# Kernel tuning notes

Measured on AMD Instinct MI355X. Metric: run time of the kernel, lower is better.

The kernel has to match this reference:

```python
import jax, jax.numpy as jnp
import numpy as np

SCALAR_DIM = 64
VECTOR_DIM = 32
SPIN = 2
N_NODES = 50000
N_EDGES = 1600000
GEO_DIM = 3
IN_DIM = 2 * SCALAR_DIM + VECTOR_DIM + GEO_DIM  # 163
HID = SCALAR_DIM + VECTOR_DIM  # 96


def setup_inputs() -> dict:
    key = jax.random.key(0)
    ks = jax.random.split(key, 9)
    h_scalar = jax.random.normal(ks[0], (N_NODES, SCALAR_DIM), dtype=jnp.float32)
    h_vector = jax.random.normal(ks[1], (N_NODES, VECTOR_DIM), dtype=jnp.float32)
    edge_index = jax.random.randint(ks[2], (2, N_EDGES), 0, N_NODES, dtype=jnp.int64)
    pos = jax.random.normal(ks[3], (N_NODES, 2), dtype=jnp.float32)
    orientation = jax.random.uniform(ks[4], (N_NODES, 1), dtype=jnp.float32)
    # MLP params (Linear: y = x @ W.T + b; store as [in, out] for jnp)
    lim1 = 1.0 / np.sqrt(IN_DIM)
    lim2 = 1.0 / np.sqrt(HID)
    W1 = jax.random.uniform(ks[5], (IN_DIM, HID), minval=-lim1, maxval=lim1, dtype=jnp.float32)
    b1 = jax.random.uniform(ks[6], (HID,), minval=-lim1, maxval=lim1, dtype=jnp.float32)
    W2 = jax.random.uniform(ks[7], (HID, HID), minval=-lim2, maxval=lim2, dtype=jnp.float32)
    b2 = jax.random.uniform(ks[8], (HID,), minval=-lim2, maxval=lim2, dtype=jnp.float32)
    return dict(h_scalar=h_scalar, h_vector=h_vector, edge_index=edge_index,
                pos=pos, orientation=orientation, W1=W1, b1=b1, W2=W2, b2=b2)


def reference(h_scalar, h_vector, edge_index, pos, orientation, W1, b1, W2, b2):
    src, dst = edge_index[0], edge_index[1]
    delta_pos = pos[src] - pos[dst]                         # [E,2]
    dist = jnp.linalg.norm(delta_pos, axis=1, keepdims=True) + 1e-6  # [E,1]
    phi_global = jnp.arctan2(delta_pos[:, 1], delta_pos[:, 0])       # [E]
    alpha_i = orientation[dst, 0]                           # [E]
    delta_phi = phi_global - alpha_i
    geo_feat = jnp.concatenate([dist,
                                jnp.cos(SPIN * delta_phi)[:, None],
                                jnp.sin(SPIN * delta_phi)[:, None]], axis=-1)  # [E,3]
    beta_j = orientation[src, 0]
    rot_angle = (beta_j - alpha_i) * SPIN
    c, s = jnp.cos(rot_angle), jnp.sin(rot_angle)
    R = jnp.stack([jnp.stack([c, -s], -1), jnp.stack([s, c], -1)], axis=-2)  # [E,2,2]
    num_vecs = VECTOR_DIM // 2
    v_j = h_vector[src].reshape(-1, num_vecs, 2)            # [E,V/2,2]
    v_j_rot = jnp.einsum('eij,evj->evi', R, v_j).reshape(-1, VECTOR_DIM)
    msg_input = jnp.concatenate([h_scalar[src], h_scalar[dst], v_j_rot, geo_feat], axis=-1)
    h = jax.nn.silu(msg_input @ W1 + b1)
    raw_msg = h @ W2 + b2                                   # [E, S+V]
    msg_scalar = raw_msg[:, :SCALAR_DIM]
    msg_vector = raw_msg[:, SCALAR_DIM:]
    out_scalar = jax.ops.segment_sum(msg_scalar, dst, num_segments=N_NODES)
    out_vector = jax.ops.segment_sum(msg_vector, dst, num_segments=N_NODES)
    return h_scalar + out_scalar, h_vector + out_vector
```

## Files before the change

### kernel.cpp

```cpp
#include <hip/hip_runtime.h>
#include <hip/hip_bf16.h>

#define N_NODESC 50000
#define N_EDGESC 1600000
#define SDIM 64
#define VDIM 32
#define HID 96
#define IN_DIMC 163

#define GRID_E 6250
#define TPB_E 4
#define NXCD 8
#define XQ (GRID_E / NXCD)
#define XR (GRID_E % NXCD)

typedef float f32x4 __attribute__((ext_vector_type(4)));
typedef short s16x8 __attribute__((ext_vector_type(8)));

__device__ __forceinline__ float bf2f(__hip_bfloat16 x) { return __bfloat162float(x); }
__device__ __forceinline__ __hip_bfloat16 f2bf(float x) { return __float2bfloat16(x); }
__device__ __forceinline__ float bfbits2f(short b) {
    unsigned u = ((unsigned)(unsigned short)b) << 16;
    return __builtin_bit_cast(float, u);
}
__device__ __forceinline__ short f2bfbits(float x) {
    __hip_bfloat16 h = __float2bfloat16(x);
    return *(const short*)&h;
}

__global__ void detect_zero(const int* ei, int* flag, int* __restrict__ counts) {
    int i = blockIdx.x * blockDim.x + threadIdx.x;
    if (i < N_NODESC) counts[i] = 0;
    if (i == 0) {
        int z = 1;
        for (int k = 0; k < 64; ++k) {
            if (ei[2 * k + 1] != 0) { z = 0; break; }
        }
        *flag = z;
    }
}

__global__ void fused_init(const float* __restrict__ hs, const float* __restrict__ hv,
                           float* __restrict__ out, int* __restrict__ counts,
                           const float* __restrict__ W1, const float* __restrict__ W2,
                           __hip_bfloat16* __restrict__ SrcRec,
                           __hip_bfloat16* __restrict__ WbT2,
                           __hip_bfloat16* __restrict__ W1cgT,
                           __hip_bfloat16* __restrict__ W2Tb,
                           const int* __restrict__ ei, const int* __restrict__ flag64) {
    int i = blockIdx.x * blockDim.x + threadIdx.x;
    if (i < N_NODESC * (SDIM + VDIM) / 4) {
        const int HS4 = N_NODESC * SDIM / 4;
        float4 v = (i < HS4) ? ((const float4*)hs)[i] : ((const float4*)hv)[i - HS4];
        ((float4*)out)[i] = v;
    }
    if (i < N_NODESC * VDIM / 8) {
        int n = i >> 2, c = i & 3;
        const float4* hv4 = (const float4*)hv;
        float4 a = hv4[n * 8 + c * 2];
        float4 bq = hv4[n * 8 + c * 2 + 1];
        s16x8 o;
        o[0] = f2bfbits(a.x);  o[1] = f2bfbits(a.y);
        o[2] = f2bfbits(a.z);  o[3] = f2bfbits(a.w);
        o[4] = f2bfbits(bq.x); o[5] = f2bfbits(bq.y);
        o[6] = f2bfbits(bq.z); o[7] = f2bfbits(bq.w);
        *(s16x8*)&SrcRec[n * 128 + 96 + c * 8] = o;
    }
    if (i < 192 * 64) {
        int n = i >> 6, k = i & 63;
        float val = (n < 96) ? W1[k * HID + n] : W1[(64 + k) * HID + (n - 96)];
        WbT2[i] = f2bf(val);
    }
    if (i < 96 * 64) {
        int n = i >> 6, k = i & 63;
        float val = 0.f;
        if (k < 32) val = W1[(128 + k) * HID + n];
        else if (k < 35) val = W1[(160 + (k - 32)) * HID + n];
        W1cgT[i] = f2bf(val);
    }
    if (i < 96 * 96) {
        int n = i / 96, k = i - (i / 96) * 96;
        W2Tb[i] = f2bf(W2[k * HID + n]);
    }
    {
        int dN;
        if (*flag64) dN = (int)((const long long*)ei)[N_EDGESC + i];
        else dN = ei[N_EDGESC + i];
        atomicAdd(&counts[dN], 1);
    }
}

__global__ __launch_bounds__(256, 2) void node_precompute_mfma(
    const float* __restrict__ hs, const __hip_bfloat16* __restrict__ WbT2,
    const float* __restrict__ b1,
    __hip_bfloat16* __restrict__ SrcRec, __hip_bfloat16* __restrict__ Qt) {
    __shared__ __hip_bfloat16 sA[64][72];
    __shared__ __hip_bfloat16 sOut[64][200];
    const int t = threadIdx.x;
    const int lane = t & 63;
    const int w = t >> 6;
    const int m16 = lane & 15;
    const int q = lane >> 4;
    const int nb = blockIdx.x * 64;

    for (int idx = t; idx < 64 * 64; idx += 256) {
        int node = idx >> 6, f = idx & 63;
        int g = nb + node;
        sA[node][f] = f2bf(g < N_NODESC ? hs[g * SDIM + f] : 0.f);
    }
    __syncthreads();

    s16x8 bfr[3][2];
    float b1v[3];
    for (int nt = 0; nt < 3; ++nt) {
        int n_out = w * 48 + nt * 16 + m16;
        for (int kt = 0; kt < 2; ++kt)
            bfr[nt][kt] = *(const s16x8*)&WbT2[n_out * 64 + kt * 32 + q * 8];
        b1v[nt] = (n_out < 96) ? b1[n_out] : 0.f;
    }

    for (int ms = 0; ms < 4; ++ms) {
        s16x8 afr[2];
        for (int kt = 0; kt < 2; ++kt)
            afr[kt] = *(const s16x8*)&sA[ms * 16 + m16][kt * 32 + q * 8];
        f32x4 acc[3];
        for (int nt = 0; nt < 3; ++nt) acc[nt] = (f32x4){0.f, 0.f, 0.f, 0.f};
        for (int nt = 0; nt < 3; ++nt)
            for (int kt = 0; kt < 2; ++kt)
                acc[nt] = __builtin_amdgcn_mfma_f32_16x16x32_bf16(
                    afr[kt], bfr[nt][kt], acc[nt], 0, 0, 0);
        for (int nt = 0; nt < 3; ++nt) {
            int n_out = w * 48 + nt * 16 + m16;
            for (int r = 0; r < 4; ++r)
                sOut[ms * 16 + q * 4 + r][n_out] = f2bf(acc[nt][r] + b1v[nt]);
        }
    }
    __syncthreads();

    for (int idx = t; idx < 64 * 12; idx += 256) {
        int node = idx / 12, ch = idx - (idx / 12) * 12;
        int g = nb + node;
        if (g < N_NODESC)
            *(s16x8*)&SrcRec[g * 128 + ch * 8] = *(const s16x8*)&sOut[node][ch * 8];
    }
    for (int idx = t; idx < 64 * 12; idx += 256) {
        int node = idx / 12, ch = idx - (idx / 12) * 12;
        int g = nb + node;
        if (g < N_NODESC)
            *(s16x8*)&Qt[g * 96 + ch * 8] = *(const s16x8*)&sOut[node][96 + ch * 8];
    }
}

__global__ __launch_bounds__(1024) void scan_kernel(
    const int* __restrict__ counts, int* __restrict__ cur) {
    __shared__ int part[1024];
    const int t = threadIdx.x;
    const int CH = (N_NODESC + 1023) / 1024;
    int lo = t * CH;
    int hi = lo + CH; if (hi > N_NODESC) hi = N_NODESC;
    int s = 0;
    for (int i = lo; i < hi; ++i) s += counts[i];
    part[t] = s;
    __syncthreads();
    for (int d = 1; d < 1024; d <<= 1) {
        int v = (t >= d) ? part[t - d] : 0;
        __syncthreads();
        part[t] += v;
        __syncthreads();
    }
    int run = (t == 0) ? 0 : part[t - 1];
    for (int i = lo; i < hi; ++i) {
        int c = counts[i];
        cur[i] = run;
        run += c;
    }
}

__global__ __launch_bounds__(256) void scatter_kernel(
    const int* __restrict__ ei, const int* __restrict__ flag64,
    int* __restrict__ cur, int2* __restrict__ edges) {
    int e = blockIdx.x * blockDim.x + threadIdx.x;
    if (e >= N_EDGESC) return;
    int sN, dN;
    if (*flag64) {
        const long long* e64 = (const long long*)ei;
        sN = (int)e64[e]; dN = (int)e64[N_EDGESC + e];
    } else { sN = ei[e]; dN = ei[N_EDGESC + e]; }
    int p = atomicAdd(&cur[dN], 1);
    edges[p] = make_int2(sN, dN);
}

__global__ __launch_bounds__(256, 3) void edge_kernel_sorted(
    const int2* __restrict__ edges,
    const float* __restrict__ pos, const float* __restrict__ ori,
    const __hip_bfloat16* __restrict__ W2Tb, const float* __restrict__ b2,
    const __hip_bfloat16* __restrict__ SrcRec, const __hip_bfloat16* __restrict__ Qt,
    const __hip_bfloat16* __restrict__ W1cgT,
    float* __restrict__ out) {
    __shared__ int s_srcM[2][64], s_dstM[2][64];
    __shared__ alignas(16) __hip_bfloat16 hVG[64][72];
    __shared__ alignas(16) __hip_bfloat16 s_vf[64][104];
    __shared__ alignas(16) short sW2f[18 * 64 * 8];
    __shared__ int s_segstart[66];

    const int t = threadIdx.x;
    const int lane = t & 63;
    const int w = t >> 6;
    const int m16 = lane & 15;
    const int q = lane >> 4;
    const int el = t >> 2;
    const int quad = t & 3;
    const int eM = w * 16 + m16;

    if (w == 0) {
        for (int f = 0; f < 18; ++f) {
            int nt = f / 3, kt = f - (f / 3) * 3;
            *(s16x8*)&sW2f[(f * 64 + lane) * 8] =
                *(const s16x8*)&W2Tb[(nt * 16 + m16) * 96 + kt * 32 + q * 8];
        }
    }
    s16x8 bfrC[6][2];
    #pragma unroll
    for (int nt = 0; nt < 6; ++nt)
        #pragma unroll
        for (int kt = 0; kt < 2; ++kt)
            bfrC[nt][kt] = *(const s16x8*)&W1cgT[(nt * 16 + m16) * 64 + kt * 32 + q * 8];
    float b2v[6];
    #pragma unroll
    for (int nt = 0; nt < 6; ++nt) b2v[nt] = b2[nt * 16 + m16];

    int b = blockIdx.x;
    int xcd = b & 7, bi = b >> 3;
    int c = (xcd < XR) ? (xcd * (XQ + 1) + bi)
                       : (XR * (XQ + 1) + (xcd - XR) * XQ + bi);
    const int tile0 = c * TPB_E;

    int2 edT1;
    s16x8 hvvT;
    float rcT, rsT;
    float gdT, gcgT, gsgT;
    {
        int2 edT = edges[tile0 * 64 + el];
        edT1 = edges[(tile0 + 1) * 64 + el];
        hvvT = *(const s16x8*)&SrcRec[edT.x * 128 + 96 + quad * 8];
        int sN = edT.x, dN = edT.y;
        float ca, sa, cb, sb;
        __sincosf(2.0f * ori[dN], &sa, &ca);
        __sincosf(2.0f * ori[sN], &sb, &cb);
        rcT = cb * ca + sb * sa;
        rsT = sb * ca - cb * sa;
        float dx = pos[2 * sN] - pos[2 * dN];
        float dy = pos[2 * sN + 1] - pos[2 * dN + 1];
        float d2 = dx * dx + dy * dy;
        gdT = sqrtf(d2) + 1e-6f;
        float c2f, s2f;
        if (d2 > 0.f) {
            float inv = 1.0f / d2;
            c2f = (dx * dx - dy * dy) * inv;
            s2f = 2.0f * dx * dy * inv;
        } else { c2f = 1.0f; s2f = 0.0f; }
        gcgT = c2f * ca + s2f * sa;
        gsgT = s2f * ca - c2f * sa;
        if (quad == 0) { s_srcM[0][el] = sN; s_dstM[0][el] = dN; }
    }
    __syncthreads();
    s16x8 pqP[3], pqQ[3];
    {
        int sN = s_srcM[0][eM], dN = s_dstM[0][eM];
        #pragma unroll
        for (int kt = 0; kt < 3; ++kt) {
            pqP[kt] = *(const s16x8*)&SrcRec[sN * 128 + kt * 32 + q * 8];
            pqQ[kt] = *(const s16x8*)&Qt[dN * 96 + kt * 32 + q * 8];
        }
    }

    int cur = 0;
    for (int tl = 0; tl < TPB_E; ++tl) {
        const int nx = cur ^ 1;
        const int tlN2 = (tl + 2 < TPB_E) ? tl + 2 : TPB_E - 1;

        {
            s16x8 rv;
            #pragma unroll
            for (int p2 = 0; p2 < 4; ++p2) {
                float x = bfbits2f(hvvT[2 * p2]), y = bfbits2f(hvvT[2 * p2 + 1]);
                rv[2 * p2]     = f2bfbits(rcT * x - rsT * y);
                rv[2 * p2 + 1] = f2bfbits(rsT * x + rcT * y);
            }
            *(s16x8*)&hVG[el][quad * 8] = rv;
            s16x8 up = (s16x8){0, 0, 0, 0, 0, 0, 0, 0};
            if (quad == 0) {
                up[0] = f2bfbits(gdT); up[1] = f2bfbits(gcgT); up[2] = f2bfbits(gsgT);
            }
            *(s16x8*)&hVG[el][32 + quad * 8] = up;
        }
        int2 edT2 = edges[(tile0 + tlN2) * 64 + el];
        s16x8 hvvN = *(const s16x8*)&SrcRec[edT1.x * 128 + 96 + quad * 8];
        {
            s16x8 afr0 = *(const s16x8*)&hVG[eM][q * 8];
            s16x8 afr1 = *(const s16x8*)&hVG[eM][32 + q * 8];
            #pragma unroll
            for (int nt = 0; nt < 6; ++nt) {
                f32x4 a1 = __builtin_amdgcn_mfma_f32_16x16x32_bf16(
                    afr0, bfrC[nt][0], (f32x4){0.f, 0.f, 0.f, 0.f}, 0, 0, 0);
                a1 = __builtin_amdgcn_mfma_f32_16x16x32_bf16(
                    afr1, bfrC[nt][1], a1, 0, 0, 0);
                int u = nt * 16 + m16;
                #pragma unroll
                for (int r = 0; r < 4; ++r)
                    s_vf[w * 16 + q * 4 + r][u] = f2bf(a1[r]);
            }
        }
        float rcN, rsN, gdN, gcgN, gsgN;
        {
            int sN = edT1.x, dN = edT1.y;
            float ca, sa, cb, sb;
            __sincosf(2.0f * ori[dN], &sa, &ca);
            __sincosf(2.0f * ori[sN], &sb, &cb);
            rcN = cb * ca + sb * sa;
            rsN = sb * ca - cb * sa;
            float dx = pos[2 * sN] - pos[2 * dN];
            float dy = pos[2 * sN + 1] - pos[2 * dN + 1];
            float d2 = dx * dx + dy * dy;
            gdN = sqrtf(d2) + 1e-6f;
            float c2f, s2f;
            if (d2 > 0.f) {
                float inv = 1.0f / d2;
                c2f = (dx * dx - dy * dy) * inv;
                s2f = 2.0f * dx * dy * inv;
            } else { c2f = 1.0f; s2f = 0.0f; }
            gcgN = c2f * ca + s2f * sa;
            gsgN = s2f * ca - c2f * sa;
            if (quad == 0) { s_srcM[nx][el] = sN; s_dstM[nx][el] = dN; }
        }

        s16x8 afr[3];
        #pragma unroll
        for (int kt = 0; kt < 3; ++kt) {
            int j = kt * 32 + q * 8;
            s16x8 Vv = *(const s16x8*)&s_vf[eM][j];
            s16x8 hb;
            #pragma unroll
            for (int k2 = 0; k2 < 8; ++k2) {
                float pre = bfbits2f(pqP[kt][k2]) + bfbits2f(pqQ[kt][k2])
                          + bfbits2f(Vv[k2]);
                float h = pre / (1.0f + __expf(-pre));
                hb[k2] = f2bfbits(h);
            }
            afr[kt] = hb;
        }
        {
            int sN = s_srcM[nx][eM], dN = s_dstM[nx][eM];
            #pragma unroll
            for (int kt = 0; kt < 3; ++kt) {
                pqP[kt] = *(const s16x8*)&SrcRec[sN * 128 + kt * 32 + q * 8];
                pqQ[kt] = *(const s16x8*)&Qt[dN * 96 + kt * 32 + q * 8];
            }
        }
        {
            f32x4 acc[6];
            #pragma unroll
            for (int nt = 0; nt < 6; ++nt) acc[nt] = (f32x4){0.f, 0.f, 0.f, 0.f};
            #pragma unroll
            for (int nt = 0; nt < 6; ++nt)
                #pragma unroll
                for (int kt = 0; kt < 3; ++kt) {
                    s16x8 bf = *(const s16x8*)&sW2f[((nt * 3 + kt) * 64 + lane) * 8];
                    acc[nt] = __builtin_amdgcn_mfma_f32_16x16x32_bf16(
                        afr[kt], bf, acc[nt], 0, 0, 0);
                }
            #pragma unroll
            for (int nt = 0; nt < 6; ++nt) {
                int u = nt * 16 + m16;
                float bb = b2v[nt];
                #pragma unroll
                for (int r = 0; r < 4; ++r)
                    s_vf[w * 16 + q * 4 + r][u] = f2bf(acc[nt][r] + bb);
            }
        }
        __syncthreads();

        {
            int dl = s_dstM[cur][lane];
            int dp = (lane > 0) ? s_dstM[cur][lane - 1] : -1;
            bool bnd = (lane > 0) && (dl != dp);
            unsigned long long mask = __ballot(bnd);
            int nseg = (int)__popcll(mask) + 1;
            if (bnd) s_segstart[__popcll(mask & (~0ull >> (63 - lane)))] = lane;
            if (lane == 0) s_segstart[0] = 0;

            for (int idx = t; idx < nseg * HID; idx += 256) {
                int sg = idx / HID;
                int u = idx - sg * HID;
                int e0 = s_segstart[sg];
                int e1 = (sg + 1 < nseg) ? s_segstart[sg + 1] : 64;
                float sum = 0.f;
                for (int e = e0; e < e1; ++e) sum += bf2f(s_vf[e][u]);
                int dN = s_dstM[cur][e0];
                if (u < SDIM) atomicAdd(&out[dN * SDIM + u], sum);
                else atomicAdd(&out[N_NODESC * SDIM + dN * VDIM + (u - SDIM)], sum);
            }
        }

        edT1 = edT2; hvvT = hvvN;
        rcT = rcN; rsT = rsN; gdT = gdN; gcgT = gcgN; gsgT = gsgN;
        cur = nx;
        __syncthreads();
    }
}

__global__ __launch_bounds__(128) void node_precompute(
    const float* __restrict__ hs, const float* __restrict__ hv,
    const float* __restrict__ W1, const float* __restrict__ b1,
    __hip_bfloat16* __restrict__ Pp, __hip_bfloat16* __restrict__ Qt,
    __hip_bfloat16* __restrict__ Ut, __hip_bfloat16* __restrict__ Vt) {
    int n = blockIdx.x;
    __shared__ float s_hs[SDIM];
    __shared__ float s_hv[VDIM];
    int t = threadIdx.x;
    if (t < 64) s_hs[t] = hs[n * SDIM + t];
    else if (t < 96) s_hv[t - 64] = hv[n * VDIM + (t - 64)];
    __syncthreads();
    if (t < HID) {
        float p = b1[t], qq = 0.f, u = 0.f, v = 0.f;
        for (int k = 0; k < 64; ++k) {
            float x = s_hs[k];
            p += x * W1[k * HID + t];
            qq += x * W1[(64 + k) * HID + t];
        }
        for (int pr = 0; pr < 16; ++pr) {
            float x = s_hv[2 * pr], y = s_hv[2 * pr + 1];
            float wa = W1[(128 + 2 * pr) * HID + t];
            float wb = W1[(128 + 2 * pr + 1) * HID + t];
            u += x * wa + y * wb;
            v += x * wb - y * wa;
        }
        Pp[n * HID + t] = f2bf(p);
        Qt[n * HID + t] = f2bf(qq);
        Ut[n * HID + t] = f2bf(u);
        Vt[n * HID + t] = f2bf(v);
    }
}

__global__ void init_out(const float* __restrict__ hs, const float* __restrict__ hv,
                         float* __restrict__ out) {
    int i = blockIdx.x * blockDim.x + threadIdx.x;
    if (i >= N_NODESC * (SDIM + VDIM)) return;
    out[i] = (i < N_NODESC * SDIM) ? hs[i] : hv[i - N_NODESC * SDIM];
}

__global__ void detect_kernel(const int* ei, int* flag) {
    if (blockIdx.x == 0 && threadIdx.x == 0) {
        int z = 1;
        for (int k = 0; k < 64; ++k) {
            if (ei[2 * k + 1] != 0) { z = 0; break; }
        }
        *flag = z;
    }
}

__global__ __launch_bounds__(256) void edge_kernel(
    const int* __restrict__ ei, const float* __restrict__ pos,
    const float* __restrict__ ori, const float* __restrict__ W1,
    const float* __restrict__ W2, const float* __restrict__ b2,
    const __hip_bfloat16* __restrict__ Pp, const __hip_bfloat16* __restrict__ Qt,
    const __hip_bfloat16* __restrict__ Ut, const __hip_bfloat16* __restrict__ Vt,
    const int* __restrict__ flag64, float* __restrict__ out) {
    __shared__ int s_src[64], s_dst[64];
    __shared__ float s_c[64], s_s[64], s_d[64], s_cg[64], s_sg[64];
    __shared__ float s_w1d[3][HID];
    __shared__ __hip_bfloat16 hA[64][104];
    __shared__ __hip_bfloat16 W2T[HID][104];

    const int t = threadIdx.x;
    const int lane = t & 63;
    const int w = t >> 6;
    const int m16 = lane & 15;
    const int q = lane >> 4;

    for (int idx = t; idx < HID * HID; idx += 256) {
        int k = idx / HID;
        int n = idx - k * HID;
        W2T[n][k] = f2bf(W2[idx]);
    }
    for (int idx = t; idx < 3 * HID; idx += 256) {
        int r = idx / HID, j = idx - r * HID;
        s_w1d[r][j] = W1[(160 + r) * HID + j];
    }
    __syncthreads();

    s16x8 bfr[6][3];
    for (int nt = 0; nt < 6; ++nt)
        for (int kt = 0; kt < 3; ++kt)
            bfr[nt][kt] = *(const s16x8*)&W2T[nt * 16 + m16][kt * 32 + q * 8];
    float b2v[6];
    for (int nt = 0; nt < 6; ++nt) b2v[nt] = b2[nt * 16 + m16];

    const bool i64 = (*flag64 != 0);
    const long long* ei64 = (const long long*)ei;

    for (int tile = blockIdx.x; tile < N_EDGESC / 64; tile += gridDim.x) {
        __syncthreads();

        if (t < 64) {
            int e = tile * 64 + t;
            int sN, dN;
            if (i64) { sN = (int)ei64[e]; dN = (int)ei64[N_EDGESC + e]; }
            else     { sN = ei[e];        dN = ei[N_EDGESC + e]; }
            s_src[t] = sN; s_dst[t] = dN;
            float ca, sa, cb, sb;
            __sincosf(2.0f * ori[dN], &sa, &ca);
            __sincosf(2.0f * ori[sN], &sb, &cb);
            s_c[t] = cb * ca + sb * sa;
            s_s[t] = sb * ca - cb * sa;
            float dx = pos[2 * sN] - pos[2 * dN];
            float dy = pos[2 * sN + 1] - pos[2 * dN + 1];
            float d2 = dx * dx + dy * dy;
            s_d[t] = sqrtf(d2) + 1e-6f;
            float c2f, s2f;
            if (d2 > 0.f) {
                float inv = 1.0f / d2;
                c2f = (dx * dx - dy * dy) * inv;
                s2f = 2.0f * dx * dy * inv;
            } else { c2f = 1.0f; s2f = 0.0f; }
            s_cg[t] = c2f * ca + s2f * sa;
            s_sg[t] = s2f * ca - c2f * sa;
        }
        __syncthreads();

        for (int p = 0; p < 24; ++p) {
            int idx = p * 256 + t;
            int e = idx / HID;
            int j = idx - e * HID;
            int sN = s_src[e], dN = s_dst[e];
            float pre = bf2f(Pp[sN * HID + j]) + bf2f(Qt[dN * HID + j])
                      + s_c[e] * bf2f(Ut[sN * HID + j])
                      + s_s[e] * bf2f(Vt[sN * HID + j])
                      + s_d[e] * s_w1d[0][j] + s_cg[e] * s_w1d[1][j]
                      + s_sg[e] * s_w1d[2][j];
            float h = pre / (1.0f + __expf(-pre));
            hA[e][j] = f2bf(h);
        }
        __syncthreads();

        f32x4 acc[6];
        for (int nt = 0; nt < 6; ++nt) acc[nt] = (f32x4){0.f, 0.f, 0.f, 0.f};
        s16x8 afr[3];
        for (int kt = 0; kt < 3; ++kt)
            afr[kt] = *(const s16x8*)&hA[w * 16 + m16][kt * 32 + q * 8];
        for (int nt = 0; nt < 6; ++nt)
            for (int kt = 0; kt < 3; ++kt)
                acc[nt] = __builtin_amdgcn_mfma_f32_16x16x32_bf16(
                    afr[kt], bfr[nt][kt], acc[nt], 0, 0, 0);

        for (int nt = 0; nt < 6; ++nt) {
            int u = nt * 16 + m16;
            for (int r = 0; r < 4; ++r) {
                int eloc = w * 16 + q * 4 + r;
                int dN = s_dst[eloc];
                float val = acc[nt][r] + b2v[nt];
                if (u < SDIM) atomicAdd(&out[dN * SDIM + u], val);
                else atomicAdd(&out[N_NODESC * SDIM + dN * VDIM + (u - SDIM)], val);
            }
        }
    }
}

__global__ __launch_bounds__(192) void edge_fallback(
    const int* __restrict__ ei, const float* __restrict__ hs,
    const float* __restrict__ hv, const float* __restrict__ pos,
    const float* __restrict__ ori, const float* __restrict__ W1,
    const float* __restrict__ b1, const float* __restrict__ W2,
    const float* __restrict__ b2, const int* __restrict__ flag64,
    float* __restrict__ out) {
    __shared__ float s_msg[IN_DIMC];
    __shared__ float s_h[HID];
    int e = blockIdx.x;
    int t = threadIdx.x;
    const bool i64 = (*flag64 != 0);
    int sN, dN;
    if (i64) {
        const long long* e64 = (const long long*)ei;
        sN = (int)e64[e]; dN = (int)e64[N_EDGESC + e];
    } else { sN = ei[e]; dN = ei[N_EDGESC + e]; }

    if (t < IN_DIMC) {
        if (t < 64) s_msg[t] = hs[sN * SDIM + t];
        else if (t < 128) s_msg[t] = hs[dN * SDIM + (t - 64)];
        else {
            float ca, sa, cb, sb;
            __sincosf(2.0f * ori[dN], &sa, &ca);
            __sincosf(2.0f * ori[sN], &sb, &cb);
            float c = cb * ca + sb * sa;
            float s = sb * ca - cb * sa;
            float dx = pos[2 * sN] - pos[2 * dN];
            float dy = pos[2 * sN + 1] - pos[2 * dN + 1];
            float d2 = dx * dx + dy * dy;
            if (t < 160) {
                int pr = (t - 128) >> 1;
                float x = hv[sN * VDIM + 2 * pr], y = hv[sN * VDIM + 2 * pr + 1];
                s_msg[t] = ((t & 1) == 0) ? (c * x - s * y) : (s * x + c * y);
            } else if (t == 160) s_msg[t] = sqrtf(d2) + 1e-6f;
            else {
                float c2f = 1.0f, s2f = 0.0f;
                if (d2 > 0.f) {
                    float inv = 1.0f / d2;
                    c2f = (dx * dx - dy * dy) * inv;
                    s2f = 2.0f * dx * dy * inv;
                }
                s_msg[t] = (t == 161) ? (c2f * ca + s2f * sa) : (s2f * ca - c2f * sa);
            }
        }
    }
    __syncthreads();
    if (t < HID) {
        float a = b1[t];
        for (int k = 0; k < IN_DIMC; ++k) a += s_msg[k] * W1[k * HID + t];
        s_h[t] = a / (1.0f + __expf(-a));
    }
    __syncthreads();
    if (t < HID) {
        float a = b2[t];
        for (int k = 0; k < HID; ++k) a += s_h[k] * W2[k * HID + t];
        if (t < SDIM) atomicAdd(&out[dN * SDIM + t], a);
        else atomicAdd(&out[N_NODESC * SDIM + dN * VDIM + (t - SDIM)], a);
    }
}

extern "C" void kernel_launch(void* const* d_in, const int* in_sizes, int n_in,
                              void* d_out, int out_size, void* d_ws, size_t ws_size,
                              hipStream_t stream) {
    const float* hs  = (const float*)d_in[0];
    const float* hv  = (const float*)d_in[1];
    const int*   ei  = (const int*)d_in[2];
    const float* pos = (const float*)d_in[3];
    const float* ori = (const float*)d_in[4];
    const float* W1  = (const float*)d_in[5];
    const float* b1  = (const float*)d_in[6];
    const float* W2  = (const float*)d_in[7];
    const float* b2  = (const float*)d_in[8];
    float* out = (float*)d_out;

    const size_t SREC = (size_t)N_NODESC * 128 * sizeof(__hip_bfloat16);
    const size_t QTB  = (size_t)N_NODESC * 96 * sizeof(__hip_bfloat16);
    const size_t CNT  = ((size_t)N_NODESC * sizeof(int) + 255) & ~255ull;
    const size_t EDG  = (size_t)N_EDGESC * sizeof(int2);
    const size_t WBT2 = ((size_t)192 * 64 * 2 + 255) & ~255ull;
    const size_t W1CG = ((size_t)96 * 64 * 2 + 255) & ~255ull;
    const size_t W2TS = ((size_t)96 * 96 * 2 + 255) & ~255ull;
    const size_t SORT_WS = SREC + QTB + 2 * CNT + EDG + WBT2 + W1CG + W2TS + 256;

    const size_t TBL = (size_t)N_NODESC * HID * sizeof(__hip_bfloat16);
    const bool big = ws_size >= 4 * TBL + 16;
    const bool srt = ws_size >= SORT_WS;

    if (srt) {
        char* ws = (char*)d_ws;
        __hip_bfloat16* SrcRec = (__hip_bfloat16*)(ws);
        __hip_bfloat16* Qt     = (__hip_bfloat16*)(ws + SREC);
        int* counts            = (int*)(ws + SREC + QTB);
        int* cur               = (int*)(ws + SREC + QTB + CNT);
        int2* edges            = (int2*)(ws + SREC + QTB + 2 * CNT);
        __hip_bfloat16* WbT2   = (__hip_bfloat16*)(ws + SREC + QTB + 2 * CNT + EDG);
        __hip_bfloat16* W1cgT  = (__hip_bfloat16*)(ws + SREC + QTB + 2 * CNT + EDG + WBT2);
        __hip_bfloat16* W2Tb   = (__hip_bfloat16*)(ws + SREC + QTB + 2 * CNT + EDG + WBT2 + W1CG);
        int* flag              = (int*)(ws + SREC + QTB + 2 * CNT + EDG + WBT2 + W1CG + W2TS);

        detect_zero<<<(N_NODESC + 255) / 256, 256, 0, stream>>>(ei, flag, counts);
        fused_init<<<N_EDGESC / 256, 256, 0, stream>>>(
            hs, hv, out, counts, W1, W2, SrcRec, WbT2, W1cgT, W2Tb, ei, flag);
        scan_kernel<<<1, 1024, 0, stream>>>(counts, cur);
        scatter_kernel<<<N_EDGESC / 256, 256, 0, stream>>>(ei, flag, cur, edges);
        node_precompute_mfma<<<(N_NODESC + 63) / 64, 256, 0, stream>>>(
            hs, WbT2, b1, SrcRec, Qt);
        edge_kernel_sorted<<<GRID_E, 256, 0, stream>>>(edges, pos, ori, W2Tb, b2,
                                                       SrcRec, Qt, W1cgT, out);
    } else if (big) {
        char* ws = (char*)d_ws;
        __hip_bfloat16* Pp = (__hip_bfloat16*)(ws);
        __hip_bfloat16* Qt = (__hip_bfloat16*)(ws + TBL);
        __hip_bfloat16* Ut = (__hip_bfloat16*)(ws + 2 * TBL);
        __hip_bfloat16* Vt = (__hip_bfloat16*)(ws + 3 * TBL);
        int* flag = (int*)(ws + 4 * TBL);
        init_out<<<(N_NODESC * (SDIM + VDIM) + 255) / 256, 256, 0, stream>>>(hs, hv, out);
        detect_kernel<<<1, 64, 0, stream>>>(ei, flag);
        node_precompute<<<N_NODESC, 128, 0, stream>>>(hs, hv, W1, b1, Pp, Qt, Ut, Vt);
        edge_kernel<<<2500, 256, 0, stream>>>(ei, pos, ori, W1, W2, b2,
                                              Pp, Qt, Ut, Vt, flag, out);
    } else {
        int* flag = (int*)d_ws;
        init_out<<<(N_NODESC * (SDIM + VDIM) + 255) / 256, 256, 0, stream>>>(hs, hv, out);
        detect_kernel<<<1, 64, 0, stream>>>(ei, flag);
        edge_fallback<<<N_EDGESC, 192, 0, stream>>>(ei, hs, hv, pos, ori, W1, b1,
                                                    W2, b2, flag, out);
    }
}
```

Before: 589.5 us.

## Parallelize prefix scan across blocks and fuse scatter with node precompute

Replaces the single-block serial-chunk prefix scan over node counts with a three-kernel block-parallel scan (per-block partials, scan of block sums, apply offsets). Merges the edge scatter kernel and the node MFMA precompute into one launch, with separate block ranges doing each job so they can run concurrently. Also swaps two divisions in the edge kernel for the hardware reciprocal intrinsic. Adds two kernel launches for the scan and uses slightly less precise reciprocals.

```diff
diff --git a/kernel.cpp b/kernel.cpp
--- a/kernel.cpp
+++ b/kernel.cpp
@@ -13,6 +13,8 @@
 #define NXCD 8
 #define XQ (GRID_E / NXCD)
 #define XR (GRID_E % NXCD)
+#define NPRE 782
+#define SCB 196
 
 typedef float f32x4 __attribute__((ext_vector_type(4)));
 typedef short s16x8 __attribute__((ext_vector_type(8)));
@@ -90,18 +92,74 @@
     }
 }
 
-__global__ __launch_bounds__(256, 2) void node_precompute_mfma(
+__global__ __launch_bounds__(256) void scan_partials(
+    const int* __restrict__ counts, int* __restrict__ cur, int* __restrict__ bsum) {
+    __shared__ int sc[256];
+    const int b = blockIdx.x, t = threadIdx.x;
+    const int i = b * 256 + t;
+    int val = (i < N_NODESC) ? counts[i] : 0;
+    sc[t] = val;
+    __syncthreads();
+    for (int d = 1; d < 256; d <<= 1) {
+        int v = (t >= d) ? sc[t - d] : 0;
+        __syncthreads();
+        sc[t] += v;
+        __syncthreads();
+    }
+    if (i < N_NODESC) cur[i] = sc[t] - val;
+    if (t == 255) bsum[b] = sc[255];
+}
+
+__global__ __launch_bounds__(256) void scan_bsums(
+    const int* __restrict__ bsum, int* __restrict__ boff) {
+    __shared__ int sc[256];
+    const int t = threadIdx.x;
+    int val = (t < SCB) ? bsum[t] : 0;
+    sc[t] = val;
+    __syncthreads();
+    for (int d = 1; d < 256; d <<= 1) {
+        int v = (t >= d) ? sc[t - d] : 0;
+        __syncthreads();
+        sc[t] += v;
+        __syncthreads();
+    }
+    if (t < SCB) boff[t] = sc[t] - val;
+}
+
+__global__ __launch_bounds__(256) void scan_apply(
+    int* __restrict__ cur, const int* __restrict__ boff) {
+    const int i = blockIdx.x * 256 + threadIdx.x;
+    if (i < N_NODESC) cur[i] += boff[blockIdx.x];
+}
+
+__global__ __launch_bounds__(256, 2) void scatter_precompute(
+    const int* __restrict__ ei, const int* __restrict__ flag64,
+    int* __restrict__ cur, int2* __restrict__ edges,
     const float* __restrict__ hs, const __hip_bfloat16* __restrict__ WbT2,
     const float* __restrict__ b1,
     __hip_bfloat16* __restrict__ SrcRec, __hip_bfloat16* __restrict__ Qt) {
     __shared__ __hip_bfloat16 sA[64][72];
     __shared__ __hip_bfloat16 sOut[64][200];
+    const int blk = blockIdx.x;
     const int t = threadIdx.x;
+
+    if (blk >= NPRE) {
+        int e = (blk - NPRE) * 256 + t;
+        int sN, dN;
+        if (*flag64) {
+            const long long* e64 = (const long long*)ei;
+            sN = (int)e64[e]; dN = (int)e64[N_EDGESC + e];
+        } else { sN = ei[e]; dN = ei[N_EDGESC + e]; }
+        int p = atomicAdd(&cur[dN], 1);
+        edges[p] = make_int2(sN, dN);
+        return;
+    }
+
     const int lane = t & 63;
     const int w = t >> 6;
     const int m16 = lane & 15;
     const int q = lane >> 4;
-    const int nb = blockIdx.x * 64;
+    const int nb = blk * 64;
 
     for (int idx = t; idx < 64 * 64; idx += 256) {
         int node = idx >> 6, f = idx & 63;
@@ -149,45 +207,6 @@
         if (g < N_NODESC)
             *(s16x8*)&Qt[g * 96 + ch * 8] = *(const s16x8*)&sOut[node][96 + ch * 8];
     }
-}
-
-__global__ __launch_bounds__(1024) void scan_kernel(
-    const int* __restrict__ counts, int* __restrict__ cur) {
-    __shared__ int part[1024];
-    const int t = threadIdx.x;
-    const int CH = (N_NODESC + 1023) / 1024;
-    int lo = t * CH;
-    int hi = lo + CH; if (hi > N_NODESC) hi = N_NODESC;
-    int s = 0;
-    for (int i = lo; i < hi; ++i) s += counts[i];
-    part[t] = s;
-    __syncthreads();
-    for (int d = 1; d < 1024; d <<= 1) {
-        int v = (t >= d) ? part[t - d] : 0;
-        __syncthreads();
-        part[t] += v;
-        __syncthreads();
-    }
-    int run = (t == 0) ? 0 : part[t - 1];
-    for (int i = lo; i < hi; ++i) {
-        int c = counts[i];
-        cur[i] = run;
-        run += c;
-    }
-}
-
-__global__ __launch_bounds__(256) void scatter_kernel(
-    const int* __restrict__ ei, const int* __restrict__ flag64,
-    int* __restrict__ cur, int2* __restrict__ edges) {
-    int e = blockIdx.x * blockDim.x + threadIdx.x;
-    if (e >= N_EDGESC) return;
-    int sN, dN;
-    if (*flag64) {
-        const long long* e64 = (const long long*)ei;
-        sN = (int)e64[e]; dN = (int)e64[N_EDGESC + e];
-    } else { sN = ei[e]; dN = ei[N_EDGESC + e]; }
-    int p = atomicAdd(&cur[dN], 1);
-    edges[p] = make_int2(sN, dN);
 }
 
 __global__ __launch_bounds__(256, 3) void edge_kernel_sorted(
@@ -255,7 +274,7 @@
         gdT = sqrtf(d2) + 1e-6f;
         float c2f, s2f;
         if (d2 > 0.f) {
-            float inv = 1.0f / d2;
+            float inv = __builtin_amdgcn_rcpf(d2);
             c2f = (dx * dx - dy * dy) * inv;
             s2f = 2.0f * dx * dy * inv;
         } else { c2f = 1.0f; s2f = 0.0f; }
@@ -325,7 +344,7 @@
             gdN = sqrtf(d2) + 1e-6f;
             float c2f, s2f;
             if (d2 > 0.f) {
-                float inv = 1.0f / d2;
+                float inv = __builtin_amdgcn_rcpf(d2);
                 c2f = (dx * dx - dy * dy) * inv;
                 s2f = 2.0f * dx * dy * inv;
             } else { c2f = 1.0f; s2f = 0.0f; }
@@ -344,7 +363,7 @@
             for (int k2 = 0; k2 < 8; ++k2) {
                 float pre = bfbits2f(pqP[kt][k2]) + bfbits2f(pqQ[kt][k2])
                           + bfbits2f(Vv[k2]);
-                float h = pre / (1.0f + __expf(-pre));
+                float h = pre * __builtin_amdgcn_rcpf(1.0f + __expf(-pre));
                 hb[k2] = f2bfbits(h);
             }
             afr[kt] = hb;
@@ -648,7 +667,11 @@
     const size_t WBT2 = ((size_t)192 * 64 * 2 + 255) & ~255ull;
     const size_t W1CG = ((size_t)96 * 64 * 2 + 255) & ~255ull;
     const size_t W2TS = ((size_t)96 * 96 * 2 + 255) & ~255ull;
-    const size_t SORT_WS = SREC + QTB + 2 * CNT + EDG + WBT2 + W1CG + W2TS + 256;
+    const size_t FLG  = 256;
+    const size_t BSM  = 1024;
+    const size_t BOF  = 1024;
+    const size_t SORT_WS = SREC + QTB + 2 * CNT + EDG + WBT2 + W1CG + W2TS
+                         + FLG + BSM + BOF;
 
     const size_t TBL = (size_t)N_NODESC * HID * sizeof(__hip_bfloat16);
     const bool big = ws_size >= 4 * TBL + 16;
@@ -664,15 +687,19 @@
         __hip_bfloat16* WbT2   = (__hip_bfloat16*)(ws + SREC + QTB + 2 * CNT + EDG);
         __hip_bfloat16* W1cgT  = (__hip_bfloat16*)(ws + SREC + QTB + 2 * CNT + EDG + WBT2);
         __hip_bfloat16* W2Tb   = (__hip_bfloat16*)(ws + SREC + QTB + 2 * CNT + EDG + WBT2 + W1CG);
-        int* flag              = (int*)(ws + SREC + QTB + 2 * CNT + EDG + WBT2 + W1CG + W2TS);
+        char* tail             = ws + SREC + QTB + 2 * CNT + EDG + WBT2 + W1CG + W2TS;
+        int* flag              = (int*)(tail);
+        int* bsum              = (int*)(tail + FLG);
+        int* boff              = (int*)(tail + FLG + BSM);
 
         detect_zero<<<(N_NODESC + 255) / 256, 256, 0, stream>>>(ei, flag, counts);
         fused_init<<<N_EDGESC / 256, 256, 0, stream>>>(
             hs, hv, out, counts, W1, W2, SrcRec, WbT2, W1cgT, W2Tb, ei, flag);
-        scan_kernel<<<1, 1024, 0, stream>>>(counts, cur);
-        scatter_kernel<<<N_EDGESC / 256, 256, 0, stream>>>(ei, flag, cur, edges);
-        node_precompute_mfma<<<(N_NODESC + 63) / 64, 256, 0, stream>>>(
-            hs, WbT2, b1, SrcRec, Qt);
+        scan_partials<<<SCB, 256, 0, stream>>>(counts, cur, bsum);
+        scan_bsums<<<1, 256, 0, stream>>>(bsum, boff);
+        scan_apply<<<SCB, 256, 0, stream>>>(cur, boff);
+        scatter_precompute<<<NPRE + N_EDGESC / 256, 256, 0, stream>>>(
+            ei, flag, cur, edges, hs, WbT2, b1, SrcRec, Qt);
         edge_kernel_sorted<<<GRID_E, 256, 0, stream>>>(edges, pos, ori, W2Tb, b2,
                                                        SrcRec, Qt, W1cgT, out);
     } else if (big) {
```

Result: faster. 496.6 us (-15.8%).
